# Optimization experiments

Measured on AMD Instinct MI355X. Metric: run time of the kernel, lower is better.

Reference implementation:

```python
import jax, jax.numpy as jnp
import numpy as np

A, B, O, C = 8, 32768, 256, 64   # num_agents, batch, obs_size, action_size
E, H = 128, 4                     # embedding_dim, attention_heads
Dh = E // H                       # attend_dim = 32
EPS = 1e-5                        # BatchNorm1d eps
SLOPE = 0.01                      # LeakyReLU default negative slope


def lrelu(x):
    return jnp.where(x >= 0, x, SLOPE * x)


def batchnorm(x, gamma, beta):
    # x: [A,B,F]; training-mode BatchNorm1d per agent (biased batch variance)
    mu = x.mean(axis=1, keepdims=True)
    var = x.var(axis=1, keepdims=True)
    return (x - mu) / jnp.sqrt(var + EPS) * gamma[:, None, :] + beta[:, None, :]


def setup_inputs() -> dict:
    key = jax.random.key(0)
    ks = jax.random.split(key, 13)
    s = lambda k, shape: jax.random.normal(k, shape, jnp.float32) * 0.05
    return {
        "observation_vector": jax.random.normal(ks[0], (A, B, O), jnp.float32),
        "action_vector": jax.random.normal(ks[1], (A, B, C), jnp.float32),
        "g_bn_gamma": jnp.ones((A, O + C), jnp.float32),
        "g_bn_beta": jnp.zeros((A, O + C), jnp.float32),
        "g_W": s(ks[2], (A, E, O + C)), "g_b": s(ks[3], (A, E)),
        "s_bn_gamma": jnp.ones((A, O), jnp.float32),
        "s_bn_beta": jnp.zeros((A, O), jnp.float32),
        "s_W": s(ks[4], (A, E, O)), "s_b": s(ks[5], (A, E)),
        "f_W1": s(ks[6], (A, E, 2 * E)), "f_b1": s(ks[7], (A, E)),
        "f_W2": s(ks[8], (A, C, E)), "f_b2": s(ks[9], (A, C)),
        "Wq": s(ks[10], (H, Dh, E)), "Wk": s(ks[11], (H, Dh, E)),
        "V": s(ks[12], (H, Dh, E)),
    }


def reference(observation_vector, action_vector, g_bn_gamma, g_bn_beta, g_W, g_b,
              s_bn_gamma, s_bn_beta, s_W, s_b, f_W1, f_b1, f_W2, f_b2, Wq, Wk, V):
    # per-agent embeddings of (obs, act) and obs-only
    combined = jnp.concatenate([observation_vector, action_vector], axis=2)      # [A,B,O+C]
    e = lrelu(jnp.einsum('abf,aef->abe', batchnorm(combined, g_bn_gamma, g_bn_beta), g_W)
              + g_b[:, None, :])                                                  # [A,B,E]
    si = lrelu(jnp.einsum('abf,aef->abe',
                          batchnorm(observation_vector, s_bn_gamma, s_bn_beta), s_W)
               + s_b[:, None, :])                                                 # [A,B,E]
    # NOTE: original applies F.softmax over a (batch,1) tensor -> every attention
    # weight is exactly 1.0, so x_i = sum_{j!=i} leaky_relu(V_l @ e_j). Wq/Wk only
    # feed the regularization logits (not returned when regularize=False).
    v = lrelu(jnp.einsum('abe,hde->abhd', e, V))                                  # [A,B,H,Dh]
    x = (v.sum(axis=0, keepdims=True) - v).reshape(A, B, E)                       # heads concatenated
    h = lrelu(jnp.einsum('abf,aef->abe', jnp.concatenate([x, si], axis=2), f_W1)
              + f_b1[:, None, :])                                                 # [A,B,E]
    q_all = jnp.einsum('abe,ace->abc', h, f_W2) + f_b2[:, None, :]                # [A,B,C]
    ids = jnp.argmax(action_vector, axis=2)[..., None]                            # [A,B,1]
    return jnp.take_along_axis(q_all, ids, axis=2)                                # [A,B,1]
```

## Files before the change

### kernel.cpp

```cpp
#include <hip/hip_runtime.h>
#include <hip/hip_bf16.h>
#include <stdint.h>

constexpr int A_ = 8, B_ = 32768, O_ = 256, C_ = 64, F_ = 320, E_ = 128;
constexpr int NCH = 128, CHROWS = B_ / NCH;
constexpr int NBT = B_ / 16;

typedef __attribute__((ext_vector_type(8))) __bf16 bf16x8;
typedef __attribute__((ext_vector_type(4))) float f32x4;
union U4 { uint4 u; bf16x8 v; __bf16 b[8]; };

__device__ __forceinline__ float lrelu(float x){ return x >= 0.f ? x : 0.01f*x; }
__device__ __forceinline__ f32x4 mfma16(bf16x8 a, bf16x8 b, f32x4 c){
  return __builtin_amdgcn_mfma_f32_16x16x32_bf16(a, b, c, 0, 0, 0);
}
__device__ __forceinline__ bf16x8 pk8(f32x4 lo, f32x4 hi){
  U4 r;
  r.b[0]=(__bf16)lo[0]; r.b[1]=(__bf16)lo[1]; r.b[2]=(__bf16)lo[2]; r.b[3]=(__bf16)lo[3];
  r.b[4]=(__bf16)hi[0]; r.b[5]=(__bf16)hi[1]; r.b[6]=(__bf16)hi[2]; r.b[7]=(__bf16)hi[3];
  return r.v;
}
__device__ __forceinline__ bf16x8 pk8f(float4 a, float4 b){
  U4 r;
  r.b[0]=(__bf16)a.x; r.b[1]=(__bf16)a.y; r.b[2]=(__bf16)a.z; r.b[3]=(__bf16)a.w;
  r.b[4]=(__bf16)b.x; r.b[5]=(__bf16)b.y; r.b[6]=(__bf16)b.z; r.b[7]=(__bf16)b.w;
  return r.v;
}
__device__ __forceinline__ void gl_lds16(const void* g, void* s){
  __builtin_amdgcn_global_load_lds(
      (const __attribute__((address_space(1))) unsigned int*)g,
      (__attribute__((address_space(3))) unsigned int*)s, 16, 0, 0);
}
template<int N> __device__ __forceinline__ void vmwait(){
  asm volatile("s_waitcnt vmcnt(%0)" :: "n"(N) : "memory");
}
__device__ __forceinline__ void lgkm0(){ asm volatile("s_waitcnt lgkmcnt(0)" ::: "memory"); }
__device__ __forceinline__ void sbar(){ __builtin_amdgcn_s_barrier(); }
__device__ __forceinline__ void schb(){ __builtin_amdgcn_sched_barrier(0); }

__global__ void k_stats_partial(const float* __restrict__ obs,
                                const float* __restrict__ act,
                                float* __restrict__ psum, float* __restrict__ psq,
                                int* __restrict__ ids){
  const int f = threadIdx.x, ch = blockIdx.x, a = blockIdx.y;
  const size_t b0 = (size_t)ch * CHROWS;
  float s = 0.f, q = 0.f;
  if (f < O_){
    const float* p = obs + ((size_t)a*B_ + b0)*O_ + f;
    for (int i = 0; i < CHROWS; ++i){ float x = p[(size_t)i*O_]; s += x; q += x*x; }
  } else {
    const float* p = act + ((size_t)a*B_ + b0)*C_ + (f - O_);
    for (int i = 0; i < CHROWS; ++i){ float x = p[(size_t)i*C_]; s += x; q += x*x; }
  }
  psum[((size_t)a*NCH + ch)*F_ + f] = s;
  psq [((size_t)a*NCH + ch)*F_ + f] = q;
  if (f < CHROWS){
    const float4* ar = (const float4*)(act + ((size_t)a*B_ + b0 + f)*C_);
    float best = -3.4e38f; int bi = 0;
    #pragma unroll 4
    for (int j = 0; j < 16; ++j){
      const float4 v = ar[j];
      const int c0 = j*4;
      if (v.x > best){ best = v.x; bi = c0;   }
      if (v.y > best){ best = v.y; bi = c0+1; }
      if (v.z > best){ best = v.z; bi = c0+2; }
      if (v.w > best){ best = v.w; bi = c0+3; }
    }
    ids[(size_t)a*B_ + b0 + f] = bi;
  }
}

__global__ void k_stats_final(const float* __restrict__ psum, const float* __restrict__ psq,
                              float* __restrict__ zscale, float* __restrict__ zshift){
  const int f = threadIdx.x, a = blockIdx.x;
  float s = 0.f, q = 0.f;
  for (int ch = 0; ch < NCH; ++ch){
    s += psum[((size_t)a*NCH + ch)*F_ + f];
    q += psq [((size_t)a*NCH + ch)*F_ + f];
  }
  const float mean = s * (1.0f / B_);
  float var = q * (1.0f / B_) - mean * mean;
  var = fmaxf(var, 0.0f);
  const float rs = rsqrtf(var + 1e-5f);
  zscale[a*F_ + f] = rs;
  zshift[a*F_ + f] = -mean * rs;
}

__global__ void k_prep_pack(const float* __restrict__ gW, const float* __restrict__ ggam,
                            const float* __restrict__ sW, const float* __restrict__ sgam,
                            const float* __restrict__ f1W, const float* __restrict__ f2W,
                            const float* __restrict__ Vm, const float* __restrict__ zscale,
                            __bf16* __restrict__ Ap, __bf16* __restrict__ Vp,
                            __bf16* __restrict__ B1p, __bf16* __restrict__ B2p){
  const int a = blockIdx.y;
  const int t0 = blockIdx.x*256 + threadIdx.x;
  constexpr int STR = 32*256;
  for (int i = t0; i < 10*16*64*8; i += STR){
    const int ks = i >> 13, mO = (i>>9)&15, l = (i>>3)&63, e = i&7;
    const int lg = l>>4, fo = mO*16 + (l&15), k = ks*32 + lg*8 + e;
    const float sc = zscale[a*F_ + k];
    float v;
    if (fo < 128) v = gW[(size_t)a*E_*F_ + (size_t)fo*F_ + k] * ggam[a*F_+k] * sc;
    else          v = (k < O_) ? sW[(size_t)a*E_*O_ + (size_t)(fo-128)*O_ + k] * sgam[a*O_+k] * sc : 0.f;
    Ap[(size_t)a*(10*16*64*8) + i] = (__bf16)v;
  }
  for (int i = t0; i < 8*8*64*8; i += STR){
    const int ks = i >> 12, mH = (i>>9)&7, l = (i>>3)&63, e = i&7;
    const int lg = l>>4, h = mH*16 + (l&15);
    const int f = 32*ks + 16*(e>>2) + 4*lg + (e&3);
    B1p[(size_t)a*(8*8*64*8) + i] = (__bf16)f1W[(size_t)a*E_*2*E_ + (size_t)h*2*E_ + f];
  }
  for (int i = t0; i < 4*4*64*8; i += STR){
    const int ks = i >> 11, mC = (i>>9)&3, l = (i>>3)&63, e = i&7;
    const int lg = l>>4, c = mC*16 + (l&15);
    const int f = 32*ks + 16*(e>>2) + 4*lg + (e&3);
    B2p[(size_t)a*(4*4*64*8) + i] = (__bf16)f2W[(size_t)a*C_*E_ + (size_t)c*E_ + f];
  }
  if (a == 0){
    for (int i = t0; i < 4*8*64*8; i += STR){
      const int ks = i >> 12, mV = (i>>9)&7, l = (i>>3)&63, e = i&7;
      const int lg = l>>4, vo = mV*16 + (l&15);
      const int f = 32*ks + 16*(e>>2) + 4*lg + (e&3);
      Vp[i] = (__bf16)Vm[(size_t)vo*E_ + f];
    }
  }
}

__global__ void k_prep_bias(const float* __restrict__ gW, const float* __restrict__ gb,
                            const float* __restrict__ ggam, const float* __restrict__ gbet,
                            const float* __restrict__ sW, const float* __restrict__ sb,
                            const float* __restrict__ sgam, const float* __restrict__ sbet,
                            const float* __restrict__ zshift, float* __restrict__ gsb){
  __shared__ float ww[F_];
  __shared__ float part[2][128];
  const int a = blockIdx.y, t = threadIdx.x;
  const int o = t & 127, h = t >> 7;
  if (blockIdx.x == 0){
    for (int f = t; f < F_; f += 256)
      ww[f] = gbet[a*F_+f] + ggam[a*F_+f]*zshift[a*F_+f];
    __syncthreads();
    float s = 0.f;
    #pragma unroll 4
    for (int f = h*160; f < h*160 + 160; f += 4){
      const float4 wv = *(const float4*)&gW[(size_t)a*E_*F_ + (size_t)o*F_ + f];
      s += wv.x*ww[f] + wv.y*ww[f+1] + wv.z*ww[f+2] + wv.w*ww[f+3];
    }
    part[h][o] = s;
    __syncthreads();
    if (t < 128) gsb[a*256 + t] = gb[a*E_+t] + part[0][t] + part[1][t];
  } else {
    for (int f = t; f < O_; f += 256)
      ww[f] = sbet[a*O_+f] + sgam[a*O_+f]*zshift[a*F_+f];
    __syncthreads();
    float s = 0.f;
    #pragma unroll 4
    for (int f = h*128; f < h*128 + 128; f += 4){
      const float4 wv = *(const float4*)&sW[(size_t)a*E_*O_ + (size_t)o*O_ + f];
      s += wv.x*ww[f] + wv.y*ww[f+1] + wv.z*ww[f+2] + wv.w*ww[f+3];
    }
    part[h][o] = s;
    __syncthreads();
    if (t < 128) gsb[a*256 + 128 + t] = sb[a*E_+t] + part[0][t] + part[1][t];
  }
}

__global__ __launch_bounds__(256, 2) void k_stageA(
    const float* __restrict__ obs, const float* __restrict__ act,
    const __bf16* __restrict__ Ap, const __bf16* __restrict__ Vp,
    const float* __restrict__ gsb,
    uint4* __restrict__ si_q, uint4* __restrict__ v_q){
  constexpr int BUF = 26624;
  __shared__ __align__(16) char smem[2*BUF];
  const int a = (A_-1) - blockIdx.y;
  const int t = threadIdx.x;
  const int w = t>>6, l = t&63, l15 = l&15, lg = l>>4;
  const int bt0 = ((NBT/8 - 1) - blockIdx.x)*8;
  const size_t grow0 = (size_t)a*B_ + (size_t)bt0*16;
  const char* ApA = (const char*)Ap + (size_t)a*163840;
  const int xr = t>>1, kc0 = (t&1)*2;
  const float* obsrow = obs + (grow0 + xr)*O_;
  const float* actrow = act + (grow0 + xr)*C_;

  float4 xA[4], xB[4];

  auto wstage = [&](int ks, char* buf){
    const char* src = ApA + ks*16384;
    #pragma unroll
    for (int i = 0; i < 4; ++i)
      gl_lds16(src + (w*4+i)*1024 + l*16, buf + (w*4+i)*1024);
  };
  auto xload = [&](int ks, float4* d){
    const float* s = (ks < 8) ? (obsrow + ks*32 + kc0*8) : (actrow + (ks-8)*32 + kc0*8);
    d[0] = ((const float4*)s)[0]; d[1] = ((const float4*)s)[1];
    d[2] = ((const float4*)s)[2]; d[3] = ((const float4*)s)[3];
  };
  auto xwrite = [&](char* buf, const float4* d){
    *(bf16x8*)(buf + 16384 + xr*80 + kc0*16)     = pk8f(d[0], d[1]);
    *(bf16x8*)(buf + 16384 + xr*80 + (kc0+1)*16) = pk8f(d[2], d[3]);
  };

  f32x4 acc[4][8] = {};

  wstage(0, smem); schb();
  xload(0, xA);
  vmwait<0>();
  xwrite(smem, xA);
  xload(1, xB);
  lgkm0(); sbar(); schb();

  #pragma unroll
  for (int ks = 0; ks < 10; ++ks){
    char* cur = smem + (ks&1)*BUF;
    char* nxt = smem + ((ks+1)&1)*BUF;
    if (ks+1 < 10){ wstage(ks+1, nxt); schb(); }
    if (ks+2 < 10) xload(ks+2, (ks&1) ? xB : xA);
    {
      const bf16x8* wc = (const bf16x8*)cur;
      const char* xb = cur + 16384;
      bf16x8 bfr[8];
      #pragma unroll
      for (int nt = 0; nt < 8; ++nt)
        bfr[nt] = *(const bf16x8*)(xb + (nt*16 + l15)*80 + lg*16);
      #pragma unroll
      for (int m = 0; m < 4; ++m){
        const bf16x8 af = wc[(w*4+m)*64 + l];
        #pragma unroll
        for (int nt = 0; nt < 8; ++nt)
          acc[m][nt] = mfma16(af, bfr[nt], acc[m][nt]);
      }
    }
    schb();
    if (ks <= 7)      vmwait<4>();
    else if (ks == 8) vmwait<0>();
    if (ks+1 < 10) xwrite(nxt, (ks&1) ? xA : xB);
    if (ks < 9){ lgkm0(); sbar(); schb(); }
  }

  const float* bE = gsb + a*256 + w*64 + lg*4;
  #pragma unroll
  for (int m = 0; m < 4; ++m){
    const float4 b = *(const float4*)(bE + m*16);
    #pragma unroll
    for (int nt = 0; nt < 8; ++nt){
      acc[m][nt][0] = lrelu(acc[m][nt][0] + b.x);
      acc[m][nt][1] = lrelu(acc[m][nt][1] + b.y);
      acc[m][nt][2] = lrelu(acc[m][nt][2] + b.z);
      acc[m][nt][3] = lrelu(acc[m][nt][3] + b.w);
    }
  }
  sbar();

  if (w < 2){
    #pragma unroll
    for (int jp = 0; jp < 2; ++jp){
      const int kv = 2*w + jp;
      #pragma unroll
      for (int nt = 0; nt < 8; ++nt)
        *(bf16x8*)(smem + ((kv*8 + nt)*64 + l)*16) = pk8(acc[2*jp][nt], acc[2*jp+1][nt]);
    }
  } else {
    #pragma unroll
    for (int jp = 0; jp < 2; ++jp){
      const int j = 2*(w-2) + jp;
      #pragma unroll
      for (int nt = 0; nt < 8; ++nt){
        U4 u; u.v = pk8(acc[2*jp][nt], acc[2*jp+1][nt]);
        si_q[(((size_t)a*NBT + bt0 + nt)*4 + j)*64 + l] = u.u;
      }
    }
  }
  lgkm0(); sbar(); schb();

  const uint4* Vq = (const uint4*)Vp;
  f32x4 accv[2][8] = {};
  #pragma unroll
  for (int kv = 0; kv < 4; ++kv){
    U4 a0, a1;
    a0.u = Vq[(kv*8 + w*2 + 0)*64 + l];
    a1.u = Vq[(kv*8 + w*2 + 1)*64 + l];
    bf16x8 bv[8];
    #pragma unroll
    for (int nt = 0; nt < 8; ++nt)
      bv[nt] = *(const bf16x8*)(smem + ((kv*8 + nt)*64 + l)*16);
    #pragma unroll
    for (int nt = 0; nt < 8; ++nt){
      accv[0][nt] = mfma16(a0.v, bv[nt], accv[0][nt]);
      accv[1][nt] = mfma16(a1.v, bv[nt], accv[1][nt]);
    }
  }
  #pragma unroll
  for (int nt = 0; nt < 8; ++nt){
    f32x4 lo, hi;
    #pragma unroll
    for (int e = 0; e < 4; ++e){ lo[e] = lrelu(accv[0][nt][e]); hi[e] = lrelu(accv[1][nt][e]); }
    U4 u; u.v = pk8(lo, hi);
    v_q[(((size_t)a*NBT + bt0 + nt)*4 + w)*64 + l] = u.u;
  }
}

__global__ void k_vsum(const uint4* __restrict__ v_q, uint4* __restrict__ vsum_q){
  const size_t i = (size_t)blockIdx.x*256 + threadIdx.x;
  const size_t per_a = (size_t)NBT*4*64;
  float s[8] = {0,0,0,0,0,0,0,0};
  #pragma unroll
  for (int aa = 0; aa < 8; ++aa){
    U4 u; u.u = v_q[aa*per_a + i];
    #pragma unroll
    for (int e = 0; e < 8; ++e) s[e] += (float)u.b[e];
  }
  U4 o;
  #pragma unroll
  for (int e = 0; e < 8; ++e) o.b[e] = (__bf16)s[e];
  vsum_q[i] = o.u;
}

__global__ __launch_bounds__(256, 2) void k_stageC(
    const uint4* __restrict__ v_q, const uint4* __restrict__ si_q,
    const uint4* __restrict__ vsum_q,
    const __bf16* __restrict__ B1p, const __bf16* __restrict__ B2p,
    const float* __restrict__ f1b, const float* __restrict__ f2b,
    const int* __restrict__ ids, float* __restrict__ out){
  __shared__ __align__(16) char wsm[2*8192];
  __shared__ float qs[4][64][17];
  const int a = blockIdx.y, t = threadIdx.x;
  const int w = t>>6, l = t&63, l15 = l&15, lg = l>>4;
  const int btw = blockIdx.x*8 + w*2;
  const char* B1A = (const char*)B1p + (size_t)a*65536;
  const size_t vbase = (size_t)a*NBT*4*64;

  uint4 qA[2], qB[2], sA[2], sB[2];

  auto wstage = [&](int ks, char* dst){
    const char* src = B1A + ks*8192;
    #pragma unroll
    for (int i = 0; i < 2; ++i)
      gl_lds16(src + (w*2+i)*1024 + l*16, dst + (w*2+i)*1024);
  };
  auto bload = [&](int ks, uint4* qv, uint4* sv){
    if (ks < 4){
      #pragma unroll
      for (int nt = 0; nt < 2; ++nt){
        const size_t idx = ((size_t)(btw+nt)*4 + ks)*64 + l;
        qv[nt] = v_q[vbase + idx];
        sv[nt] = vsum_q[idx];
      }
    } else {
      #pragma unroll
      for (int nt = 0; nt < 2; ++nt)
        qv[nt] = si_q[vbase + ((size_t)(btw+nt)*4 + (ks-4))*64 + l];
    }
  };
  auto bmake = [&](int ks, const uint4* qv, const uint4* sv, bf16x8* bf){
    if (ks < 4){
      #pragma unroll
      for (int nt = 0; nt < 2; ++nt){
        U4 s, v; s.u = sv[nt]; v.u = qv[nt];
        f32x4 lo, hi;
        #pragma unroll
        for (int e = 0; e < 4; ++e){
          lo[e] = (float)s.b[e]   - (float)v.b[e];
          hi[e] = (float)s.b[e+4] - (float)v.b[e+4];
        }
        bf[nt] = pk8(lo, hi);
      }
    } else {
      #pragma unroll
      for (int nt = 0; nt < 2; ++nt){ U4 u; u.u = qv[nt]; bf[nt] = u.v; }
    }
  };

  f32x4 hacc[8][2] = {};
  wstage(0, wsm); schb();
  bload(0, qA, sA); schb();
  bload(1, qB, sB);
  vmwait<4>();
  sbar(); schb();

  #pragma unroll
  for (int ks = 0; ks < 8; ++ks){
    bf16x8 bf[2];
    bmake(ks, (ks&1) ? qB : qA, (ks&1) ? sB : sA, bf);
    if (ks+1 < 8){ wstage(ks+1, wsm + ((ks+1)&1)*8192); schb(); }
    if (ks+2 < 8) bload(ks+2, (ks&1) ? qB : qA, (ks&1) ? sB : sA);
    {
      const bf16x8* wc = (const bf16x8*)(wsm + (ks&1)*8192);
      #pragma unroll
      for (int m = 0; m < 8; ++m){
        const bf16x8 af = wc[m*64 + l];
        hacc[m][0] = mfma16(af, bf[0], hacc[m][0]);
        hacc[m][1] = mfma16(af, bf[1], hacc[m][1]);
      }
    }
    schb();
    if (ks <= 1)      vmwait<4>();
    else if (ks <= 5) vmwait<2>();
    else if (ks == 6) vmwait<0>();
    if (ks < 7){ sbar(); schb(); }
  }

  bf16x8 hb[4][2];
  const float* bH = f1b + a*E_ + lg*4;
  #pragma unroll
  for (int kq = 0; kq < 4; ++kq){
    const float4 b0v = *(const float4*)(bH + (2*kq)*16);
    const float4 b1v = *(const float4*)(bH + (2*kq+1)*16);
    #pragma unroll
    for (int nt = 0; nt < 2; ++nt){
      f32x4 lo, hi;
      lo[0]=lrelu(hacc[2*kq][nt][0]+b0v.x); lo[1]=lrelu(hacc[2*kq][nt][1]+b0v.y);
      lo[2]=lrelu(hacc[2*kq][nt][2]+b0v.z); lo[3]=lrelu(hacc[2*kq][nt][3]+b0v.w);
      hi[0]=lrelu(hacc[2*kq+1][nt][0]+b1v.x); hi[1]=lrelu(hacc[2*kq+1][nt][1]+b1v.y);
      hi[2]=lrelu(hacc[2*kq+1][nt][2]+b1v.z); hi[3]=lrelu(hacc[2*kq+1][nt][3]+b1v.w);
      hb[kq][nt] = pk8(lo, hi);
    }
  }
  const uint4* A2q = (const uint4*)(B2p + (size_t)a*(4*4*64*8));
  f32x4 accq[4][2] = {};
  #pragma unroll
  for (int kq = 0; kq < 4; ++kq){
    #pragma unroll
    for (int mC = 0; mC < 4; ++mC){
      U4 af; af.u = A2q[(kq*4 + mC)*64 + l];
      accq[mC][0] = mfma16(af.v, hb[kq][0], accq[mC][0]);
      accq[mC][1] = mfma16(af.v, hb[kq][1], accq[mC][1]);
    }
  }
  const float* bQ = f2b + a*C_ + lg*4;
  float4 qb[4];
  #pragma unroll
  for (int mC = 0; mC < 4; ++mC) qb[mC] = *(const float4*)(bQ + mC*16);
  #pragma unroll
  for (int nt = 0; nt < 2; ++nt){
    #pragma unroll
    for (int mC = 0; mC < 4; ++mC){
      qs[w][mC*16 + lg*4 + 0][l15] = accq[mC][nt][0] + qb[mC].x;
      qs[w][mC*16 + lg*4 + 1][l15] = accq[mC][nt][1] + qb[mC].y;
      qs[w][mC*16 + lg*4 + 2][l15] = accq[mC][nt][2] + qb[mC].z;
      qs[w][mC*16 + lg*4 + 3][l15] = accq[mC][nt][3] + qb[mC].w;
    }
    lgkm0();
    if (l < 16){
      const size_t row = (size_t)(btw + nt)*16 + l;
      const int id = ids[(size_t)a*B_ + row];
      out[(size_t)a*B_ + row] = qs[w][id][l];
    }
    lgkm0();
  }
}

extern "C" void kernel_launch(void* const* d_in, const int* in_sizes, int n_in,
                              void* d_out, int out_size, void* d_ws, size_t ws_size,
                              hipStream_t stream) {
  const float* obs  = (const float*)d_in[0];
  const float* act  = (const float*)d_in[1];
  const float* ggam = (const float*)d_in[2];
  const float* gbet = (const float*)d_in[3];
  const float* gW   = (const float*)d_in[4];
  const float* gb   = (const float*)d_in[5];
  const float* sgam = (const float*)d_in[6];
  const float* sbet = (const float*)d_in[7];
  const float* sW   = (const float*)d_in[8];
  const float* sb   = (const float*)d_in[9];
  const float* f1W  = (const float*)d_in[10];
  const float* f1b  = (const float*)d_in[11];
  const float* f2W  = (const float*)d_in[12];
  const float* f2b  = (const float*)d_in[13];
  const float* Vm   = (const float*)d_in[16];
  float* out = (float*)d_out;

  char* base = (char*)d_ws; size_t off = 0;
  auto alloc = [&](size_t bytes) -> void* {
    off = (off + 255) & ~(size_t)255; void* p = base + off; off += bytes; return p;
  };
  float* psum    = (float*)alloc((size_t)A_*NCH*F_*4);
  float* psq     = (float*)alloc((size_t)A_*NCH*F_*4);
  float* zscale  = (float*)alloc((size_t)A_*F_*4);
  float* zshift  = (float*)alloc((size_t)A_*F_*4);
  float* gsb     = (float*)alloc((size_t)A_*256*4);
  __bf16* Ap     = (__bf16*)alloc((size_t)A_*10*16*64*8*2);
  __bf16* Vp     = (__bf16*)alloc((size_t)4*8*64*8*2);
  __bf16* B1p    = (__bf16*)alloc((size_t)A_*8*8*64*8*2);
  __bf16* B2p    = (__bf16*)alloc((size_t)A_*4*4*64*8*2);
  uint4* si_q    = (uint4*)alloc((size_t)A_*NBT*4*64*16);
  uint4* v_q     = (uint4*)alloc((size_t)A_*NBT*4*64*16);
  uint4* vsum_q  = (uint4*)alloc((size_t)NBT*4*64*16);
  int*   ids     = (int*)alloc((size_t)A_*B_*4);
  (void)ws_size; (void)in_sizes; (void)n_in; (void)out_size;

  k_stats_partial<<<dim3(NCH, A_), 320, 0, stream>>>(obs, act, psum, psq, ids);
  k_stats_final<<<A_, F_, 0, stream>>>(psum, psq, zscale, zshift);
  k_prep_pack<<<dim3(32, A_), 256, 0, stream>>>(gW, ggam, sW, sgam, f1W, f2W, Vm,
                                                zscale, Ap, Vp, B1p, B2p);
  k_prep_bias<<<dim3(2, A_), 256, 0, stream>>>(gW, gb, ggam, gbet, sW, sb, sgam, sbet,
                                               zshift, gsb);
  k_stageA<<<dim3(NBT/8, A_), 256, 0, stream>>>(obs, act, Ap, Vp, gsb, si_q, v_q);
  k_vsum<<<(NBT*4*64)/256, 256, 0, stream>>>(v_q, vsum_q);
  k_stageC<<<dim3(NBT/8, A_), 256, 0, stream>>>(v_q, si_q, vsum_q, B1p, B2p,
                                                 f1b, f2b, ids, out);
}
```

Before: 256.2 us.

## Triple-buffer stage-A pipeline, fold stats finalize into prep kernels, unroll stats loops

```diff
diff --git a/kernel.cpp b/kernel.cpp
--- a/kernel.cpp
+++ b/kernel.cpp
@@ -47,9 +47,11 @@
   float s = 0.f, q = 0.f;
   if (f < O_){
     const float* p = obs + ((size_t)a*B_ + b0)*O_ + f;
+    #pragma unroll 8
     for (int i = 0; i < CHROWS; ++i){ float x = p[(size_t)i*O_]; s += x; q += x*x; }
   } else {
     const float* p = act + ((size_t)a*B_ + b0)*C_ + (f - O_);
+    #pragma unroll 8
     for (int i = 0; i < CHROWS; ++i){ float x = p[(size_t)i*C_]; s += x; q += x*x; }
   }
   psum[((size_t)a*NCH + ch)*F_ + f] = s;
@@ -70,35 +72,33 @@
   }
 }
 
-__global__ void k_stats_final(const float* __restrict__ psum, const float* __restrict__ psq,
-                              float* __restrict__ zscale, float* __restrict__ zshift){
-  const int f = threadIdx.x, a = blockIdx.x;
-  float s = 0.f, q = 0.f;
-  for (int ch = 0; ch < NCH; ++ch){
-    s += psum[((size_t)a*NCH + ch)*F_ + f];
-    q += psq [((size_t)a*NCH + ch)*F_ + f];
-  }
-  const float mean = s * (1.0f / B_);
-  float var = q * (1.0f / B_) - mean * mean;
-  var = fmaxf(var, 0.0f);
-  const float rs = rsqrtf(var + 1e-5f);
-  zscale[a*F_ + f] = rs;
-  zshift[a*F_ + f] = -mean * rs;
-}
-
 __global__ void k_prep_pack(const float* __restrict__ gW, const float* __restrict__ ggam,
                             const float* __restrict__ sW, const float* __restrict__ sgam,
                             const float* __restrict__ f1W, const float* __restrict__ f2W,
-                            const float* __restrict__ Vm, const float* __restrict__ zscale,
+                            const float* __restrict__ Vm,
+                            const float* __restrict__ psum, const float* __restrict__ psq,
                             __bf16* __restrict__ Ap, __bf16* __restrict__ Vp,
                             __bf16* __restrict__ B1p, __bf16* __restrict__ B2p){
+  __shared__ float zs[F_];
   const int a = blockIdx.y;
   const int t0 = blockIdx.x*256 + threadIdx.x;
   constexpr int STR = 32*256;
+  for (int f = threadIdx.x; f < F_; f += 256){
+    float s = 0.f, q = 0.f;
+    for (int ch = 0; ch < NCH; ++ch){
+      s += psum[((size_t)a*NCH + ch)*F_ + f];
+      q += psq [((size_t)a*NCH + ch)*F_ + f];
+    }
+    const float mean = s * (1.0f / B_);
+    float var = q * (1.0f / B_) - mean * mean;
+    var = fmaxf(var, 0.0f);
+    zs[f] = rsqrtf(var + 1e-5f);
+  }
+  __syncthreads();
   for (int i = t0; i < 10*16*64*8; i += STR){
     const int ks = i >> 13, mO = (i>>9)&15, l = (i>>3)&63, e = i&7;
     const int lg = l>>4, fo = mO*16 + (l&15), k = ks*32 + lg*8 + e;
-    const float sc = zscale[a*F_ + k];
+    const float sc = zs[k];
     float v;
     if (fo < 128) v = gW[(size_t)a*E_*F_ + (size_t)fo*F_ + k] * ggam[a*F_+k] * sc;
     else          v = (k < O_) ? sW[(size_t)a*E_*O_ + (size_t)(fo-128)*O_ + k] * sgam[a*O_+k] * sc : 0.f;
@@ -130,14 +130,28 @@
                             const float* __restrict__ ggam, const float* __restrict__ gbet,
                             const float* __restrict__ sW, const float* __restrict__ sb,
                             const float* __restrict__ sgam, const float* __restrict__ sbet,
-                            const float* __restrict__ zshift, float* __restrict__ gsb){
+                            const float* __restrict__ psum, const float* __restrict__ psq,
+                            float* __restrict__ gsb){
   __shared__ float ww[F_];
   __shared__ float part[2][128];
   const int a = blockIdx.y, t = threadIdx.x;
   const int o = t & 127, h = t >> 7;
+  __shared__ float zsh[F_];
+  for (int f = t; f < F_; f += 256){
+    float s = 0.f, q = 0.f;
+    for (int ch = 0; ch < NCH; ++ch){
+      s += psum[((size_t)a*NCH + ch)*F_ + f];
+      q += psq [((size_t)a*NCH + ch)*F_ + f];
+    }
+    const float mean = s * (1.0f / B_);
+    float var = q * (1.0f / B_) - mean * mean;
+    var = fmaxf(var, 0.0f);
+    zsh[f] = -mean * rsqrtf(var + 1e-5f);
+  }
+  __syncthreads();
   if (blockIdx.x == 0){
     for (int f = t; f < F_; f += 256)
-      ww[f] = gbet[a*F_+f] + ggam[a*F_+f]*zshift[a*F_+f];
+      ww[f] = gbet[a*F_+f] + ggam[a*F_+f]*zsh[f];
     __syncthreads();
     float s = 0.f;
     #pragma unroll 4
@@ -150,7 +164,7 @@
     if (t < 128) gsb[a*256 + t] = gb[a*E_+t] + part[0][t] + part[1][t];
   } else {
     for (int f = t; f < O_; f += 256)
-      ww[f] = sbet[a*O_+f] + sgam[a*O_+f]*zshift[a*F_+f];
+      ww[f] = sbet[a*O_+f] + sgam[a*O_+f]*zsh[f];
     __syncthreads();
     float s = 0.f;
     #pragma unroll 4
@@ -170,7 +184,7 @@
     const float* __restrict__ gsb,
     uint4* __restrict__ si_q, uint4* __restrict__ v_q){
   constexpr int BUF = 26624;
-  __shared__ __align__(16) char smem[2*BUF];
+  __shared__ __align__(16) char smem[3*BUF];
   const int a = (A_-1) - blockIdx.y;
   const int t = threadIdx.x;
   const int w = t>>6, l = t&63, l15 = l&15, lg = l>>4;
@@ -181,7 +195,7 @@
   const float* obsrow = obs + (grow0 + xr)*O_;
   const float* actrow = act + (grow0 + xr)*C_;
 
-  float4 xA[4], xB[4];
+  float4 X0[4], X1[4], X2[4];
 
   auto wstage = [&](int ks, char* buf){
     const char* src = ApA + ks*16384;
@@ -201,19 +215,23 @@
 
   f32x4 acc[4][8] = {};
 
-  wstage(0, smem); schb();
-  xload(0, xA);
-  vmwait<0>();
-  xwrite(smem, xA);
-  xload(1, xB);
+  wstage(0, smem);
+  xload(0, X0);
+  wstage(1, smem + BUF);
+  xload(1, X1);
+  schb();
+  vmwait<20>();
+  xwrite(smem, X0);
   lgkm0(); sbar(); schb();
 
   #pragma unroll
   for (int ks = 0; ks < 10; ++ks){
-    char* cur = smem + (ks&1)*BUF;
-    char* nxt = smem + ((ks+1)&1)*BUF;
-    if (ks+1 < 10){ wstage(ks+1, nxt); schb(); }
-    if (ks+2 < 10) xload(ks+2, (ks&1) ? xB : xA);
+    float4* Xn = (ks%3==0) ? X2 : ((ks%3==1) ? X0 : X1);
+    float4* Xw = (ks%3==0) ? X1 : ((ks%3==1) ? X2 : X0);
+    char* cur = smem + (ks%3)*BUF;
+    char* nx1 = smem + ((ks+1)%3)*BUF;
+    char* nx2 = smem + ((ks+2)%3)*BUF;
+    if (ks+2 < 10){ wstage(ks+2, nx2); xload(ks+2, Xn); schb(); }
     {
       const bf16x8* wc = (const bf16x8*)cur;
       const char* xb = cur + 16384;
@@ -230,9 +248,9 @@
       }
     }
     schb();
-    if (ks <= 7)      vmwait<4>();
-    else if (ks == 8) vmwait<0>();
-    if (ks+1 < 10) xwrite(nxt, (ks&1) ? xA : xB);
+    if (ks+2 < 10)     vmwait<20>();
+    else if (ks == 8)  vmwait<0>();
+    if (ks+1 < 10) xwrite(nx1, Xw);
     if (ks < 9){ lgkm0(); sbar(); schb(); }
   }
 
@@ -474,8 +492,6 @@
   };
   float* psum    = (float*)alloc((size_t)A_*NCH*F_*4);
   float* psq     = (float*)alloc((size_t)A_*NCH*F_*4);
-  float* zscale  = (float*)alloc((size_t)A_*F_*4);
-  float* zshift  = (float*)alloc((size_t)A_*F_*4);
   float* gsb     = (float*)alloc((size_t)A_*256*4);
   __bf16* Ap     = (__bf16*)alloc((size_t)A_*10*16*64*8*2);
   __bf16* Vp     = (__bf16*)alloc((size_t)4*8*64*8*2);
@@ -488,11 +504,10 @@
   (void)ws_size; (void)in_sizes; (void)n_in; (void)out_size;
 
   k_stats_partial<<<dim3(NCH, A_), 320, 0, stream>>>(obs, act, psum, psq, ids);
-  k_stats_final<<<A_, F_, 0, stream>>>(psum, psq, zscale, zshift);
   k_prep_pack<<<dim3(32, A_), 256, 0, stream>>>(gW, ggam, sW, sgam, f1W, f2W, Vm,
-                                                zscale, Ap, Vp, B1p, B2p);
+                                                psum, psq, Ap, Vp, B1p, B2p);
   k_prep_bias<<<dim3(2, A_), 256, 0, stream>>>(gW, gb, ggam, gbet, sW, sb, sgam, sbet,
-                                               zshift, gsb);
+                                               psum, psq, gsb);
   k_stageA<<<dim3(NBT/8, A_), 256, 0, stream>>>(obs, act, Ap, Vp, gsb, si_q, v_q);
   k_vsum<<<(NBT*4*64)/256, 256, 0, stream>>>(v_q, vsum_q);
   k_stageC<<<dim3(NBT/8, A_), 256, 0, stream>>>(v_q, si_q, vsum_q, B1p, B2p,
```

Result: slower. 280.4 us (+9.4%).
